# Optimization experiments

Measured on AMD Instinct MI355X. Metric: run time of the kernel, lower is better.

The kernel has to match this reference:

```python
import jax, jax.numpy as jnp
import numpy as np

H = 256      # hidden_size
B = 32       # batch
T = 4096     # timesteps / graph nodes
E = 8192     # edges per graph
PATH = 1
EXPAND_WEIGHT = 0.1
MODE = 'son'


def setup_inputs() -> dict:
    key = jax.random.key(0)
    ks = jax.random.split(key, 6)
    hidden = jax.random.normal(ks[0], (B, H), jnp.float32)
    encoder_outputs = jax.random.normal(ks[1], (T, B, H), jnp.float32)
    edges_src = jax.random.randint(ks[2], (B, E), 0, T)
    edges_dst = jax.random.randint(ks[3], (B, E), 0, T)
    # nn.Linear(2H, 2H) params (kaiming-uniform-ish scale) and the v vector
    lim = 1.0 / np.sqrt(2 * H)
    W_attn = jax.random.uniform(ks[4], (2 * H, 2 * H), jnp.float32, -lim, lim)
    b_attn = jnp.zeros((2 * H,), jnp.float32)
    v = jax.random.uniform(ks[5], (2 * H,), jnp.float32, -lim, lim)
    return {"hidden": hidden, "encoder_outputs": encoder_outputs,
            "edges_src": edges_src, "edges_dst": edges_dst,
            "W_attn": W_attn, "b_attn": b_attn, "v": v}


def reference(hidden, encoder_outputs, edges_src, edges_dst, W_attn, b_attn, v):
    Bb, Hh = hidden.shape
    Tt = encoder_outputs.shape[0]
    # h: [B, T, H] (hidden repeated over timesteps); enc: [B, T, H]
    h = jnp.broadcast_to(hidden[:, None, :], (Bb, Tt, Hh))
    enc = jnp.transpose(encoder_outputs, (1, 0, 2))
    # score: tanh(Linear(cat)) then v . energy -> [B, T]
    energy = jnp.tanh(jnp.concatenate([h, enc], axis=2) @ W_attn.T + b_attn)
    scores = jnp.einsum('btd,d->bt', energy, v)
    w = jax.nn.softmax(scores, axis=1)
    # expand_attn: scatter-add along graph edges, skipping consecutive (y == x+1)
    mask = (edges_dst != edges_src + 1).astype(w.dtype)  # [B, E]
    def scatter(wb, src, dst, m):
        if MODE == 'son':
            return jnp.zeros_like(wb).at[dst].add(wb[src] * m)
        else:
            return jnp.zeros_like(wb).at[src].add(wb[dst] * m)
    for _ in range(PATH):
        w = jax.vmap(scatter)(w, edges_src, edges_dst, mask) * EXPAND_WEIGHT
    return w[:, None, :]  # [B, 1, T]
```

## Files before the change

### kernel.cpp

```cpp
#include <hip/hip_runtime.h>
#include <hip/hip_bf16.h>

typedef __attribute__((ext_vector_type(8))) short bf16x8;
typedef __attribute__((ext_vector_type(4))) float f32x4;

#define HD 256
#define NB 32
#define NT 4096
#define NE 8192
#define N2 512

static __device__ __forceinline__ unsigned short f2bf(float f) {
  unsigned int u = __float_as_uint(f);
  u += 0x7fff + ((u >> 16) & 1);
  return (unsigned short)(u >> 16);
}
static __device__ __forceinline__ short4 cvt4(float4 a) {
  return make_short4((short)f2bf(a.x), (short)f2bf(a.y),
                     (short)f2bf(a.z), (short)f2bf(a.w));
}
static __device__ __forceinline__ float fast_tanh(float x) {
  x = fminf(15.f, fmaxf(-15.f, x));
  float e = __expf(x + x);
  return (e - 1.f) * __builtin_amdgcn_rcpf(e + 1.f);
}

__global__ __launch_bounds__(256) void prep(
    const float* __restrict__ hidden, const float* __restrict__ Wattn,
    const float* __restrict__ battn, float* __restrict__ cvecT,
    short* __restrict__ Wbf) {
  const int tid = threadIdx.x;
  if (blockIdx.x < 256) {
    __shared__ float Ws[64 * 260];
    __shared__ float Hs[HD];
    const int chunk = blockIdx.x & 7;
    const int b = blockIdx.x >> 3;
#pragma unroll
    for (int it = 0; it < 16; ++it) {
      int f = it * 1024 + tid * 4;
      int i = f >> 8, k = f & 255;
      float4 w4 = *(const float4*)(Wattn + (chunk * 64 + i) * N2 + k);
      *(float4*)&Ws[i * 260 + k] = w4;
    }
    if (tid < 64)
      *(float4*)&Hs[tid * 4] = *(const float4*)(hidden + b * HD + tid * 4);
    __syncthreads();
    const int nl = tid >> 2;
    const int kb = (tid & 3) * 64;
    float sum = 0.f;
#pragma unroll
    for (int z = 0; z < 64; z += 4) {
      float4 h4 = *(const float4*)&Hs[kb + z];
      float4 w4 = *(const float4*)&Ws[nl * 260 + kb + z];
      sum = fmaf(h4.x, w4.x, sum);
      sum = fmaf(h4.y, w4.y, sum);
      sum = fmaf(h4.z, w4.z, sum);
      sum = fmaf(h4.w, w4.w, sum);
    }
    sum += __shfl_xor(sum, 1, 64);
    sum += __shfl_xor(sum, 2, 64);
    if ((tid & 3) == 0)
      cvecT[(chunk * 64 + nl) * NB + b] = sum + battn[chunk * 64 + nl];
  } else {
    int f = (blockIdx.x - 256) * 1024 + tid * 4;
    int n = f >> 8, k = f & 255;
    float4 w4 = *(const float4*)(Wattn + n * N2 + HD + k);
    *(short4*)(Wbf + f) = cvt4(w4);
  }
}

__global__ __launch_bounds__(256, 2) void score_gemm(
    const float* __restrict__ enc, const short* __restrict__ Wbf,
    const float* __restrict__ cvecT, const float* __restrict__ vvec,
    float* __restrict__ scores) {
  __shared__ short As[128 * 256];
  __shared__ float part[4][128];
  const int tid = threadIdx.x;
  const int w = tid >> 6, lane = tid & 63, q = lane >> 4, m = lane & 15;
  const long row0 = (long)blockIdx.x * 128;

  ((float*)part)[tid] = 0.f;
  ((float*)part)[tid + 256] = 0.f;

  const float* src = enc + row0 * HD;
#pragma unroll
  for (int it = 0; it < 32; ++it) {
    int f = it * 1024 + tid * 4;
    float4 a4 = *(const float4*)(src + f);
    int r = f >> 8, k = f & 255;
    int slot = (k >> 3) ^ (r & 31);
    *(short4*)&As[(r * 32 + slot) * 8 + (k & 7)] = cvt4(a4);
  }
  __syncthreads();

#pragma unroll 1
  for (int cc = 0; cc < 2; ++cc) {
    const int nb = cc * 256 + w * 64;
    bf16x8 breg[4][8];
    float vv[4];
    float4 cv[4][2];
#pragma unroll
    for (int c = 0; c < 4; ++c) {
      const int n = nb + c * 16 + m;
      const short* bp = Wbf + n * HD + q * 8;
#pragma unroll
      for (int kk = 0; kk < 8; ++kk) breg[c][kk] = *(const bf16x8*)(bp + kk * 32);
      vv[c] = vvec[n];
      cv[c][0] = *(const float4*)(cvecT + n * NB + q * 4);
      cv[c][1] = *(const float4*)(cvecT + n * NB + 16 + q * 4);
    }
#pragma unroll 1
    for (int rt = 0; rt < 8; ++rt) {
      const int r = rt * 16 + m;
      const int rx = r & 31;
      f32x4 acc[4] = {{0.f,0.f,0.f,0.f},{0.f,0.f,0.f,0.f},
                      {0.f,0.f,0.f,0.f},{0.f,0.f,0.f,0.f}};
#pragma unroll
      for (int kk = 0; kk < 8; ++kk) {
        bf16x8 a = *(const bf16x8*)&As[(r * 32 + ((kk * 4 + q) ^ rx)) * 8];
#pragma unroll
        for (int c = 0; c < 4; ++c)
          acc[c] = __builtin_amdgcn_mfma_f32_16x16x32_bf16(a, breg[c][kk], acc[c], 0, 0, 0);
      }
      const int p = rt & 1;
#pragma unroll
      for (int j = 0; j < 4; ++j) {
        float e = fast_tanh(acc[0][j] + cv[0][p][j]) * vv[0]
                + fast_tanh(acc[1][j] + cv[1][p][j]) * vv[1]
                + fast_tanh(acc[2][j] + cv[2][p][j]) * vv[2]
                + fast_tanh(acc[3][j] + cv[3][p][j]) * vv[3];
        e += __shfl_xor(e, 1, 64);
        e += __shfl_xor(e, 2, 64);
        e += __shfl_xor(e, 4, 64);
        e += __shfl_xor(e, 8, 64);
        if (m == 0) part[w][rt * 16 + 4 * q + j] += e;
      }
    }
  }
  __syncthreads();
  if (tid < 128) {
    const long r = row0 + tid;
    scores[(r & 31) * NT + (r >> 5)] =
        part[0][tid] + part[1][tid] + part[2][tid] + part[3][tid];
  }
}

__global__ __launch_bounds__(1024) void softmax_norm(
    float* __restrict__ sc, float* __restrict__ out) {
  __shared__ float rtmp[16];
  __shared__ float rres;
  const int b = blockIdx.x;
  const int tid = threadIdx.x;
  const int wid = tid >> 6, lane = tid & 63;
  float s[4];
  float mx = -1e30f;
#pragma unroll
  for (int p = 0; p < 4; ++p) {
    s[p] = sc[b * NT + tid + p * 1024];
    mx = fmaxf(mx, s[p]);
  }
#pragma unroll
  for (int d = 32; d >= 1; d >>= 1) mx = fmaxf(mx, __shfl_xor(mx, d, 64));
  if (lane == 0) rtmp[wid] = mx;
  __syncthreads();
  if (tid == 0) {
    float mm = rtmp[0];
#pragma unroll
    for (int i = 1; i < 16; ++i) mm = fmaxf(mm, rtmp[i]);
    rres = mm;
  }
  __syncthreads();
  mx = rres;
  float sm = 0.f;
#pragma unroll
  for (int p = 0; p < 4; ++p) {
    s[p] = __expf(s[p] - mx);
    sm += s[p];
  }
#pragma unroll
  for (int d = 32; d >= 1; d >>= 1) sm += __shfl_xor(sm, d, 64);
  if (lane == 0) rtmp[wid] = sm;
  __syncthreads();
  if (tid == 0) {
    float tt = 0.f;
#pragma unroll
    for (int i = 0; i < 16; ++i) tt += rtmp[i];
    rres = tt;
  }
  __syncthreads();
  const float scale = 0.1f / rres;
#pragma unroll
  for (int p = 0; p < 4; ++p) {
    int i = tid + p * 1024;
    sc[b * NT + i] = s[p] * scale;
    out[b * NT + i] = 0.f;
  }
}

__global__ __launch_bounds__(512) void scatter(
    const float* __restrict__ wn, const int* __restrict__ esrc,
    const int* __restrict__ edst, float* __restrict__ out) {
  const int b = blockIdx.x >> 4;
  const int e = (blockIdx.x & 15) * 512 + threadIdx.x;
  const int ss = esrc[b * NE + e];
  const int dd = edst[b * NE + e];
  if (dd != ss + 1) atomicAdd(out + b * NT + dd, wn[b * NT + ss]);
}

extern "C" void kernel_launch(void* const* d_in, const int* in_sizes, int n_in,
                              void* d_out, int out_size, void* d_ws, size_t ws_size,
                              hipStream_t stream) {
  const float* hidden = (const float*)d_in[0];
  const float* enc    = (const float*)d_in[1];
  const int*   esrc   = (const int*)d_in[2];
  const int*   edst   = (const int*)d_in[3];
  const float* Wattn  = (const float*)d_in[4];
  const float* battn  = (const float*)d_in[5];
  const float* vvec   = (const float*)d_in[6];
  float* out = (float*)d_out;

  char* ws = (char*)d_ws;
  float* cvecT  = (float*)ws;
  short* Wbf    = (short*)(ws + 65536);
  float* scores = (float*)(ws + 65536 + 262144);

  prep<<<384, 256, 0, stream>>>(hidden, Wattn, battn, cvecT, Wbf);
  score_gemm<<<(NB * NT) / 128, 256, 0, stream>>>(enc, Wbf, cvecT, vvec, scores);
  softmax_norm<<<NB, 1024, 0, stream>>>(scores, out);
  scatter<<<512, 512, 0, stream>>>(scores, esrc, edst, out);
}
```

Before: 319.5 us.

## Defer cross-lane score reduction and shrink per-wave column tile in score GEMM

Each wave now keeps per-row partial energy sums in registers across all column chunks, and does the 16-lane shuffle reduction and shared-memory write once at the end instead of after every row tile. The column chunk per wave drops from 64 to 32 columns, so fewer B fragments stay resident, and the row-tile loop is fully unrolled. The goal is to cut repeated shuffle and LDS read-modify-write traffic and to ease register pressure. In exchange B fragments are reloaded over four passes instead of two, and each MFMA pair has less independent work to hide latency.

```diff
diff --git a/kernel.cpp b/kernel.cpp
--- a/kernel.cpp
+++ b/kernel.cpp
@@ -79,9 +79,6 @@
   const int w = tid >> 6, lane = tid & 63, q = lane >> 4, m = lane & 15;
   const long row0 = (long)blockIdx.x * 128;
 
-  ((float*)part)[tid] = 0.f;
-  ((float*)part)[tid + 256] = 0.f;
-
   const float* src = enc + row0 * HD;
 #pragma unroll
   for (int it = 0; it < 32; ++it) {
@@ -93,48 +90,63 @@
   }
   __syncthreads();
 
+  float rowacc[8][4];
+#pragma unroll
+  for (int rt = 0; rt < 8; ++rt)
+#pragma unroll
+    for (int j = 0; j < 4; ++j) rowacc[rt][j] = 0.f;
+
 #pragma unroll 1
-  for (int cc = 0; cc < 2; ++cc) {
-    const int nb = cc * 256 + w * 64;
-    bf16x8 breg[4][8];
-    float vv[4];
-    float4 cv[4][2];
-#pragma unroll
-    for (int c = 0; c < 4; ++c) {
+  for (int cc = 0; cc < 4; ++cc) {
+    const int nb = cc * 128 + w * 32;
+    bf16x8 breg[2][8];
+    float vv[2];
+    f32x4 cva[2], cvb[2];
+#pragma unroll
+    for (int c = 0; c < 2; ++c) {
       const int n = nb + c * 16 + m;
       const short* bp = Wbf + n * HD + q * 8;
 #pragma unroll
       for (int kk = 0; kk < 8; ++kk) breg[c][kk] = *(const bf16x8*)(bp + kk * 32);
       vv[c] = vvec[n];
-      cv[c][0] = *(const float4*)(cvecT + n * NB + q * 4);
-      cv[c][1] = *(const float4*)(cvecT + n * NB + 16 + q * 4);
-    }
-#pragma unroll 1
+      cva[c] = *(const f32x4*)(cvecT + n * NB + q * 4);
+      cvb[c] = *(const f32x4*)(cvecT + n * NB + 16 + q * 4);
+    }
+#pragma unroll
     for (int rt = 0; rt < 8; ++rt) {
       const int r = rt * 16 + m;
       const int rx = r & 31;
-      f32x4 acc[4] = {{0.f,0.f,0.f,0.f},{0.f,0.f,0.f,0.f},
-                      {0.f,0.f,0.f,0.f},{0.f,0.f,0.f,0.f}};
+      f32x4 acc0 = {0.f, 0.f, 0.f, 0.f}, acc1 = {0.f, 0.f, 0.f, 0.f};
 #pragma unroll
       for (int kk = 0; kk < 8; ++kk) {
         bf16x8 a = *(const bf16x8*)&As[(r * 32 + ((kk * 4 + q) ^ rx)) * 8];
-#pragma unroll
-        for (int c = 0; c < 4; ++c)
-          acc[c] = __builtin_amdgcn_mfma_f32_16x16x32_bf16(a, breg[c][kk], acc[c], 0, 0, 0);
+        acc0 = __builtin_amdgcn_mfma_f32_16x16x32_bf16(a, breg[0][kk], acc0, 0, 0, 0);
+        acc1 = __builtin_amdgcn_mfma_f32_16x16x32_bf16(a, breg[1][kk], acc1, 0, 0, 0);
       }
-      const int p = rt & 1;
-#pragma unroll
-      for (int j = 0; j < 4; ++j) {
-        float e = fast_tanh(acc[0][j] + cv[0][p][j]) * vv[0]
-                + fast_tanh(acc[1][j] + cv[1][p][j]) * vv[1]
-                + fast_tanh(acc[2][j] + cv[2][p][j]) * vv[2]
-                + fast_tanh(acc[3][j] + cv[3][p][j]) * vv[3];
-        e += __shfl_xor(e, 1, 64);
-        e += __shfl_xor(e, 2, 64);
-        e += __shfl_xor(e, 4, 64);
-        e += __shfl_xor(e, 8, 64);
-        if (m == 0) part[w][rt * 16 + 4 * q + j] += e;
+      if (rt & 1) {
+#pragma unroll
+        for (int j = 0; j < 4; ++j)
+          rowacc[rt][j] += fast_tanh(acc0[j] + cvb[0][j]) * vv[0]
+                         + fast_tanh(acc1[j] + cvb[1][j]) * vv[1];
+      } else {
+#pragma unroll
+        for (int j = 0; j < 4; ++j)
+          rowacc[rt][j] += fast_tanh(acc0[j] + cva[0][j]) * vv[0]
+                         + fast_tanh(acc1[j] + cva[1][j]) * vv[1];
       }
+    }
+  }
+
+#pragma unroll
+  for (int rt = 0; rt < 8; ++rt) {
+#pragma unroll
+    for (int j = 0; j < 4; ++j) {
+      float e = rowacc[rt][j];
+      e += __shfl_xor(e, 1, 64);
+      e += __shfl_xor(e, 2, 64);
+      e += __shfl_xor(e, 4, 64);
+      e += __shfl_xor(e, 8, 64);
+      if (m == 0) part[w][rt * 16 + 4 * q + j] = e;
     }
   }
   __syncthreads();
```

After: 390.0 us. +22.1%, slower.
